# Kernel optimization log

Hardware: AMD Instinct MI355X
Metric: run time of the kernel (lower is better)

## Reference

```python
import jax, jax.numpy as jnp
import numpy as np

IMG = 800.0
STRIDES = (4, 8, 16, 32)
SIZES = (32.0, 64.0, 128.0, 256.0)
RATIOS = (0.5, 1.0, 2.0)
A = 3
PRE_NMS_K = 1000
POST_NMS = 512
NMS_TH = 0.7
POOL = 7
_MEAN = np.array([0.485, 0.456, 0.406], np.float32).reshape(3, 1, 1)
_STD = np.array([0.229, 0.224, 0.225], np.float32).reshape(3, 1, 1)


def _conv(x, w, stride=1):
    # x: [C,H,W], w: [O,I,kh,kw]
    return jax.lax.conv_general_dilated(x[None], w, (stride, stride), 'SAME',
                                        dimension_numbers=('NCHW', 'OIHW', 'NCHW'))[0]


def _make_anchors(fh, fw, stride, size):
    cy = (np.arange(fh, dtype=np.float32) + 0.5) * stride
    cx = (np.arange(fw, dtype=np.float32) + 0.5) * stride
    ws = np.array([size / np.sqrt(r) for r in RATIOS], np.float32)
    hs = np.array([size * np.sqrt(r) for r in RATIOS], np.float32)
    gy, gx = np.meshgrid(cy, cx, indexing='ij')
    x1 = gx[..., None] - ws / 2; y1 = gy[..., None] - hs / 2
    x2 = gx[..., None] + ws / 2; y2 = gy[..., None] + hs / 2
    return jnp.asarray(np.stack([x1, y1, x2, y2], -1).reshape(-1, 4))  # [fh*fw*A,4]


def _decode(anchors, deltas):
    aw = anchors[:, 2] - anchors[:, 0]; ah = anchors[:, 3] - anchors[:, 1]
    acx = anchors[:, 0] + aw * 0.5; acy = anchors[:, 1] + ah * 0.5
    dw = jnp.clip(deltas[:, 2], -4.0, 4.0); dh = jnp.clip(deltas[:, 3], -4.0, 4.0)
    cx = acx + deltas[:, 0] * aw; cy = acy + deltas[:, 1] * ah
    w = aw * jnp.exp(dw); h = ah * jnp.exp(dh)
    boxes = jnp.stack([cx - w * 0.5, cy - h * 0.5, cx + w * 0.5, cy + h * 0.5], -1)
    return jnp.clip(boxes, 0.0, IMG)


def _nms(boxes, scores, iou_th, max_out):
    # Greedy NMS with fixed output size (jit-compatible).
    x1, y1, x2, y2 = boxes[:, 0], boxes[:, 1], boxes[:, 2], boxes[:, 3]
    areas = (x2 - x1) * (y2 - y1)

    def body(i, state):
        s, keep = state
        idx = jnp.argmax(s)
        keep = keep.at[i].set(idx)
        ix1 = jnp.maximum(x1, x1[idx]); iy1 = jnp.maximum(y1, y1[idx])
        ix2 = jnp.minimum(x2, x2[idx]); iy2 = jnp.minimum(y2, y2[idx])
        inter = jnp.maximum(ix2 - ix1, 0.0) * jnp.maximum(iy2 - iy1, 0.0)
        iou = inter / (areas + areas[idx] - inter + 1e-6)
        return jnp.where(iou > iou_th, -jnp.inf, s), keep

    _, keep = jax.lax.fori_loop(0, max_out, body, (scores, jnp.zeros(max_out, jnp.int32)))
    return keep


def _roi_align(feat, rois, scale):
    # feat: [C,H,W]; rois: [N,4] in image coords; bilinear, 1 sample per bin.
    C, H, W = feat.shape
    n = rois.shape[0]
    x1 = rois[:, 0] * scale; y1 = rois[:, 1] * scale
    bw = (rois[:, 2] - rois[:, 0]) * scale / POOL
    bh = (rois[:, 3] - rois[:, 1]) * scale / POOL
    j = jnp.arange(POOL, dtype=feat.dtype) + 0.5
    gx = jnp.broadcast_to((x1[:, None] + j * bw[:, None] - 0.5)[:, None, :], (n, POOL, POOL))
    gy = jnp.broadcast_to((y1[:, None] + j * bh[:, None] - 0.5)[:, :, None], (n, POOL, POOL))
    fx = jnp.clip(jnp.floor(gx), 0.0, W - 1); fy = jnp.clip(jnp.floor(gy), 0.0, H - 1)
    x0 = fx.astype(jnp.int32); y0 = fy.astype(jnp.int32)
    x1i = jnp.minimum(x0 + 1, W - 1); y1i = jnp.minimum(y0 + 1, H - 1)
    wx = jnp.clip(gx - fx, 0.0, 1.0); wy = jnp.clip(gy - fy, 0.0, 1.0)
    v = (feat[:, y0, x0] * (1 - wy) * (1 - wx) + feat[:, y0, x1i] * (1 - wy) * wx
         + feat[:, y1i, x0] * wy * (1 - wx) + feat[:, y1i, x1i] * wy * wx)  # [C,N,P,P]
    return jnp.transpose(v, (1, 0, 2, 3))  # [N,C,P,P]


def _forward(x, stem_w, c2_w, c3_w, c4_w, c5_w, fpn2_w, fpn3_w, fpn4_w, fpn5_w,
             rpn_w, rpn_cls_w, rpn_box_w, fc1_w, fc1_b, fc2_w, fc2_b,
             cls_w, cls_b, breg_w, breg_b):
    x = (x - _MEAN) / _STD  # ImageNet normalize
    h = jax.nn.relu(_conv(x, stem_w, 2))      # [64,400,400]
    c2 = jax.nn.relu(_conv(h, c2_w, 2))       # [256,200,200] stride 4
    c3 = jax.nn.relu(_conv(c2, c3_w, 2))      # stride 8
    c4 = jax.nn.relu(_conv(c3, c4_w, 2))      # stride 16
    c5 = jax.nn.relu(_conv(c4, c5_w, 2))      # stride 32
    feats = [_conv(c2, fpn2_w), _conv(c3, fpn3_w), _conv(c4, fpn4_w), _conv(c5, fpn5_w)]

    boxes_l, scores_l = [], []
    for lvl, f in enumerate(feats):
        t = jax.nn.relu(_conv(f, rpn_w))
        fh, fw = f.shape[1], f.shape[2]
        logits = jnp.transpose(_conv(t, rpn_cls_w), (1, 2, 0)).reshape(-1)  # [fh*fw*A]
        deltas = jnp.transpose(_conv(t, rpn_box_w).reshape(A, 4, fh, fw), (2, 3, 0, 1)).reshape(-1, 4)
        anchors = _make_anchors(fh, fw, STRIDES[lvl], SIZES[lvl])
        dec = _decode(anchors, deltas)
        k = min(PRE_NMS_K, logits.shape[0])
        sc, idx = jax.lax.top_k(logits, k)
        boxes_l.append(dec[idx]); scores_l.append(sc)

    boxes = jnp.concatenate(boxes_l, 0)
    scores = jnp.concatenate(scores_l, 0)
    keep = _nms(boxes, scores, NMS_TH, POST_NMS)
    props = boxes[keep]  # [POST_NMS,4]

    pooled = _roi_align(feats[0], props, 1.0 / STRIDES[0])  # [N,256,7,7]
    v = pooled.reshape(POST_NMS, -1)
    v = jax.nn.relu(v @ fc1_w + fc1_b)
    v = jax.nn.relu(v @ fc2_w + fc2_b)
    return v @ cls_w + cls_b, v @ breg_w + breg_b, props, scores[keep]


def setup_inputs() -> dict:
    key = jax.random.key(0)
    ks = jax.random.split(key, 18)

    def he(k, shape):
        fan_in = int(np.prod(shape[1:])) if len(shape) == 4 else shape[0]
        return jax.random.normal(k, shape, jnp.float32) * float(np.sqrt(2.0 / fan_in))

    inp = {'x': jax.random.uniform(ks[0], (3, 800, 800), jnp.float32)}
    inp['stem_w'] = he(ks[1], (64, 3, 7, 7))
    inp['c2_w'] = he(ks[2], (256, 64, 3, 3))
    for i, name in enumerate(['c3_w', 'c4_w', 'c5_w', 'fpn2_w', 'fpn3_w', 'fpn4_w', 'fpn5_w', 'rpn_w']):
        inp[name] = he(ks[3 + i], (256, 256, 3, 3))
    inp['rpn_cls_w'] = he(ks[11], (3, 256, 1, 1))
    inp['rpn_box_w'] = he(ks[12], (12, 256, 1, 1))
    inp['fc1_w'] = he(ks[13], (12544, 1024)); inp['fc1_b'] = jnp.zeros((1024,), jnp.float32)
    inp['fc2_w'] = he(ks[14], (1024, 1024)); inp['fc2_b'] = jnp.zeros((1024,), jnp.float32)
    inp['cls_w'] = he(ks[15], (1024, 2)); inp['cls_b'] = jnp.zeros((2,), jnp.float32)
    inp['breg_w'] = he(ks[16], (1024, 8)); inp['breg_b'] = jnp.zeros((8,), jnp.float32)
    return inp


def reference(x, stem_w, c2_w, c3_w, c4_w, c5_w, fpn2_w, fpn3_w, fpn4_w, fpn5_w,
              rpn_w, rpn_cls_w, rpn_box_w, fc1_w, fc1_b, fc2_w, fc2_b,
              cls_w, cls_b, breg_w, breg_b):
    return _forward(x, stem_w, c2_w, c3_w, c4_w, c5_w, fpn2_w, fpn3_w, fpn4_w, fpn5_w,
                    rpn_w, rpn_cls_w, rpn_box_w, fc1_w, fc1_b, fc2_w, fc2_b,
                    cls_w, cls_b, breg_w, breg_b)
```

## Files before the change

### kernel.cpp

```cpp
#include <hip/hip_runtime.h>
#include <math.h>


#define DI __device__ __forceinline__

typedef short short8 __attribute__((ext_vector_type(8)));
typedef float float16v __attribute__((ext_vector_type(16)));

DI unsigned fkey(float f) {
  unsigned u = __float_as_uint(f);
  return (u & 0x80000000u) ? ~u : (u | 0x80000000u);
}

DI unsigned short f2bf(float f) {
  unsigned u = __float_as_uint(f);
  unsigned r = (u + 0x7FFFu + ((u >> 16) & 1u)) >> 16;
  return (unsigned short)r;
}

DI void rp256(const float* src, float* dst, int j) {
  int co = j & 15; int r = j >> 4; int kk = r % 9; int r2 = r / 9;
  int ci = r2 & 255; int z = r2 >> 8;
  dst[j] = src[((size_t)(z * 16 + co) * 256 + ci) * 9 + kk];
}
// ... 49 lines not shown
  const int tid = threadIdx.x;
  const int ix0 = x0 * 2 - 2, iy0 = y0 * 2 - 2;
  const float mean[3] = {0.485f, 0.456f, 0.406f};
  const float stdv[3] = {0.229f, 0.224f, 0.225f};
  for (int i = tid; i < 3 * 37 * 37; i += 256) {
    int c = i / 1369, r = i % 1369, yy = r / 37, xx = r % 37;
    int gy = iy0 + yy, gx = ix0 + xx;
    float v = 0.f;
    if ((unsigned)gy < 800u && (unsigned)gx < 800u)
      v = __fdiv_rn(__fsub_rn(x[c * 640000 + gy * 800 + gx], mean[c]), stdv[c]);
    tin[i] = v;
  }
  __syncthreads();
  const int tx = tid & 15, ty = tid >> 4;
  float acc[4] = {0.f, 0.f, 0.f, 0.f};
  const float4* wq = (const float4*)(wpkS + (size_t)blockIdx.z * 588);
  for (int c = 0; c < 3; ++c)
    for (int ky = 0; ky < 7; ++ky)
#pragma unroll
      for (int kx = 0; kx < 7; ++kx) {
        float v = tin[c * 1369 + (ty * 2 + ky) * 37 + (tx * 2 + kx)];
        float4 wv = wq[c * 49 + ky * 7 + kx];
        acc[0] = fmaf(v, wv.x, acc[0]);
        acc[1] = fmaf(v, wv.y, acc[1]);
        acc[2] = fmaf(v, wv.z, acc[2]);
        acc[3] = fmaf(v, wv.w, acc[3]);
      }
  int ox = x0 + tx, oy = y0 + ty;
#pragma unroll
  for (int co = 0; co < 4; ++co)
    out[(size_t)(co0 + co) * 160000 + oy * 400 + ox] = fmaxf(acc[co], 0.f);
}

template <int CHUNK, bool RELU>
DI void conv32_body(const float* __restrict__ in,
                    const float* __restrict__ wpk, float* __restrict__ out,
                    int Cin, int Hin, int Win, int Hout, int Wout, int bx,
                    int by, int bz, float (*tin2)[((CHUNK * 612 + 255) / 256) * 256]) {
  constexpr int TILE = CHUNK * 612;
  constexpr int NS = (TILE + 255) / 256;
  const int tid = threadIdx.x;
  const int tx = tid & 15, ty = tid >> 4;
  const int x0 = bx * 32, y0 = by * 16;
  const int ix0 = x0 - 1, iy0 = y0 - 1;
  const size_t HWin = (size_t)Hin * Win;

  int goff[NS];
#pragma unroll
  for (int j = 0; j < NS; ++j) {
    int e = j * 256 + tid;
    int c = e / 612, r = e % 612;
    int yy = r / 34, xx = r % 34;
    int gy = iy0 + yy, gx = ix0 + xx;
    bool ok = (e < TILE) && ((unsigned)gy < (unsigned)Hin) &&
              ((unsigned)gx < (unsigned)Win);
    goff[j] = ok ? (int)((size_t)c * HWin + (size_t)gy * Win + gx) : -1;
  }

  float acc0[16], acc1[16];
#pragma unroll
  for (int co = 0; co < 16; ++co) { acc0[co] = 0.f; acc1[co] = 0.f; }

  float stg[NS];
#pragma unroll
  for (int j = 0; j < NS; ++j)
    stg[j] = (goff[j] >= 0) ? in[goff[j]] : 0.f;
#pragma unroll
  for (int j = 0; j < NS; ++j) tin2[0][j * 256 + tid] = stg[j];
  __syncthreads();

  int buf = 0;
// ... 39 lines not shown
          acc1[6]  = fmaf(v1, w1.z, acc1[6]);
          acc1[7]  = fmaf(v1, w1.w, acc1[7]);
          acc0[8]  = fmaf(v0, w2.x, acc0[8]);
          acc0[9]  = fmaf(v0, w2.y, acc0[9]);
          acc0[10] = fmaf(v0, w2.z, acc0[10]);
          acc0[11] = fmaf(v0, w2.w, acc0[11]);
          acc1[8]  = fmaf(v1, w2.x, acc1[8]);
          acc1[9]  = fmaf(v1, w2.y, acc1[9]);
          acc1[10] = fmaf(v1, w2.z, acc1[10]);
          acc1[11] = fmaf(v1, w2.w, acc1[11]);
          acc0[12] = fmaf(v0, w3.x, acc0[12]);
          acc0[13] = fmaf(v0, w3.y, acc0[13]);
          acc0[14] = fmaf(v0, w3.z, acc0[14]);
          acc0[15] = fmaf(v0, w3.w, acc0[15]);
          acc1[12] = fmaf(v1, w3.x, acc1[12]);
          acc1[13] = fmaf(v1, w3.y, acc1[13]);
          acc1[14] = fmaf(v1, w3.z, acc1[14]);
          acc1[15] = fmaf(v1, w3.w, acc1[15]);
        }
      }
    }
    if (more) {
#pragma unroll
      for (int j = 0; j < NS; ++j) tin2[buf ^ 1][j * 256 + tid] = stg[j];
    }
    __syncthreads();
    buf ^= 1;
  }

  const int co0 = bz * 16;
  int oy = y0 + ty;
  if (oy < Hout) {
    int ox = x0 + 2 * tx;
    if (ox + 1 < Wout) {
#pragma unroll
      for (int co = 0; co < 16; ++co) {
        float a = acc0[co], b = acc1[co];
        if (RELU) { a = fmaxf(a, 0.f); b = fmaxf(b, 0.f); }
        float2 st; st.x = a; st.y = b;
        *(float2*)&out[(size_t)(co0 + co) * Hout * Wout +
                       (size_t)oy * Wout + ox] = st;
      }
    } else if (ox < Wout) {
#pragma unroll
      for (int co = 0; co < 16; ++co) {
        float a = acc0[co];
        if (RELU) a = fmaxf(a, 0.f);
        out[(size_t)(co0 + co) * Hout * Wout + (size_t)oy * Wout + ox] = a;
      }
    }
  }
}

template <int CHUNK, bool RELU>
__global__ __launch_bounds__(256) void conv32_db(
    const float* __restrict__ in, const float* __restrict__ wpk,
    float* __restrict__ out, int Cin, int Hin, int Win, int Hout, int Wout) {
  constexpr int PADT = ((CHUNK * 612 + 255) / 256) * 256;
  __shared__ __align__(16) float tin2[2][PADT];
  conv32_body<CHUNK, RELU>(in, wpk, out, Cin, Hin, Win, Hout, Wout,
                           blockIdx.x, blockIdx.y, blockIdx.z, tin2);
}

template <int CHUNK>
__global__ __launch_bounds__(256) void conv32_lat(
    const float* __restrict__ inA, const float* __restrict__ wA,
    float* __restrict__ oA, int CinA, int HA, int WA, int gxA, int gyA,
    int nA, const float* __restrict__ inB, const float* __restrict__ wB,
    float* __restrict__ oB, int CinB, int HB, int WB, int gxB, int gyB) {
  constexpr int PADT = ((CHUNK * 612 + 255) / 256) * 256;
  __shared__ __align__(16) float tin2[2][PADT];
  int bid = blockIdx.x;
  if (bid < nA) {
    int bx = bid % gxA; int r = bid / gxA; int by = r % gyA; int bz = r / gyA;
    conv32_body<CHUNK, false>(inA, wA, oA, CinA, HA, WA, HA, WA, bx, by, bz,
                              tin2);
  } else {
    bid -= nA;
    int bx = bid % gxB; int r = bid / gxB; int by = r % gyB; int bz = r / gyB;
    conv32_body<CHUNK, false>(inB, wB, oB, CinB, HB, WB, HB, WB, bx, by, bz,
                              tin2);
  }
}

template <int CHUNK, bool RELU>
DI void conv16s1_body(const float* __restrict__ in,
                      const float* __restrict__ wpk, float* __restrict__ out,
                      int Cin, int Hin, int Win, int Hout, int Wout, int bx,
                      int by, int bz, float* tin) {
  constexpr int P = 24;
  constexpr int TOT = CHUNK * 18 * 18;
  constexpr int NS = (TOT + 255) / 256;
  const int tid = threadIdx.x;
  const int tx = tid & 15, ty = tid >> 4;
  const int x0 = bx * 16, y0 = by * 16;
  const int ix0 = x0 - 1, iy0 = y0 - 1;
  const size_t HWin = (size_t)Hin * Win;

  int goff[NS], loff[NS];
#pragma unroll
  for (int j = 0; j < NS; ++j) {
    int i = tid + j * 256;
    int c = i / 324, r = i % 324;
    int yy = r / 18, xx = r % 18;
    int gy = iy0 + yy, gx = ix0 + xx;
    bool ok = (i < TOT) && ((unsigned)gy < (unsigned)Hin) &&
              ((unsigned)gx < (unsigned)Win);
    goff[j] = ok ? (int)(c * HWin + (size_t)gy * Win + gx) : -1;
    loff[j] = c * 18 * P + yy * P + xx;
  }

  float acc[16];
#pragma unroll
  for (int co = 0; co < 16; ++co) acc[co] = 0.f;

  for (int cb = 0; cb < Cin; cb += CHUNK) {
    const size_t gbase = (size_t)cb * HWin;
#pragma unroll
// ... 13 lines not shown
      for (int ky = 0; ky < 3; ++ky) {
#pragma unroll
        for (int kx = 0; kx < 3; ++kx) {
          const int kk = ky * 3 + kx;
          float v = tin[ci * 18 * P + (ty + ky) * P + tx + kx];
          float4 w0 = wq[kk * 4 + 0];
          float4 w1 = wq[kk * 4 + 1];
          float4 w2 = wq[kk * 4 + 2];
          float4 w3 = wq[kk * 4 + 3];
          acc[0]  = fmaf(v, w0.x, acc[0]);
          acc[1]  = fmaf(v, w0.y, acc[1]);
          acc[2]  = fmaf(v, w0.z, acc[2]);
          acc[3]  = fmaf(v, w0.w, acc[3]);
          acc[4]  = fmaf(v, w1.x, acc[4]);
          acc[5]  = fmaf(v, w1.y, acc[5]);
          acc[6]  = fmaf(v, w1.z, acc[6]);
          acc[7]  = fmaf(v, w1.w, acc[7]);
          acc[8]  = fmaf(v, w2.x, acc[8]);
          acc[9]  = fmaf(v, w2.y, acc[9]);
          acc[10] = fmaf(v, w2.z, acc[10]);
          acc[11] = fmaf(v, w2.w, acc[11]);
          acc[12] = fmaf(v, w3.x, acc[12]);
          acc[13] = fmaf(v, w3.y, acc[13]);
          acc[14] = fmaf(v, w3.z, acc[14]);
          acc[15] = fmaf(v, w3.w, acc[15]);
        }
      }
    }
    __syncthreads();
  }
  const int co0 = bz * 16;
  int oy = y0 + ty, ox = x0 + tx;
  if (oy < Hout && ox < Wout) {
#pragma unroll
    for (int co = 0; co < 16; ++co) {
      float v = acc[co];
      if (RELU) v = fmaxf(v, 0.f);
      out[(size_t)(co0 + co) * Hout * Wout + (size_t)oy * Wout + ox] = v;
    }
  }
}

template <int CHUNK, bool RELU>
__global__ __launch_bounds__(256) void conv16_s1(const float* __restrict__ in,
                                                 const float* __restrict__ wpk,
                                                 float* __restrict__ out,
                                                 int Cin, int Hin, int Win,
                                                 int Hout, int Wout) {
  __shared__ __align__(16) float tin[CHUNK * 18 * 24];
  conv16s1_body<CHUNK, RELU>(in, wpk, out, Cin, Hin, Win, Hout, Wout,
                             blockIdx.x, blockIdx.y, blockIdx.z, tin);
}

template <int CHUNK>
__global__ __launch_bounds__(256) void conv16_lat(
    const float* __restrict__ inA, const float* __restrict__ wA,
    float* __restrict__ oA, int CinA, int HA, int WA, int gxA, int gyA,
    int nA, const float* __restrict__ inB, const float* __restrict__ wB,
    float* __restrict__ oB, int CinB, int HB, int WB, int gxB, int gyB) {
  __shared__ __align__(16) float tin[CHUNK * 18 * 24];
  int bid = blockIdx.x;
  if (bid < nA) {
    int bx = bid % gxA; int r = bid / gxA; int by = r % gyA; int bz = r / gyA;
    conv16s1_body<CHUNK, false>(inA, wA, oA, CinA, HA, WA, HA, WA, bx, by, bz,
                                tin);
  } else {
    bid -= nA;
    int bx = bid % gxB; int r = bid / gxB; int by = r % gyB; int bz = r / gyB;
    conv16s1_body<CHUNK, false>(inB, wB, oB, CinB, HB, WB, HB, WB, bx, by, bz,
                                tin);
  }
}

template <int CHUNK, bool RELU>
__global__ __launch_bounds__(256) void conv16_s2(const float* __restrict__ in,
                                                 const float* __restrict__ wpk,
                                                 float* __restrict__ out,
                                                 int Cin, int Hin, int Win,
                                                 int Hout, int Wout) {
  constexpr int P = 20;
  constexpr int HALF = CHUNK * 33 * P;
  constexpr int TOT = CHUNK * 33 * 33;
  constexpr int NS = (TOT + 255) / 256;
  __shared__ __align__(16) float tin2[2 * HALF];
  const int tid = threadIdx.x;
  const int tx = tid & 15, ty = tid >> 4;
  const int x0 = blockIdx.x * 16, y0 = blockIdx.y * 16;
  const int ix0 = x0 * 2, iy0 = y0 * 2;
  const size_t HWin = (size_t)Hin * Win;

  int goff[NS], loff[NS];
#pragma unroll
  for (int j = 0; j < NS; ++j) {
    int i = tid + j * 256;
    int c = i / 1089, r = i % 1089;
    int yy = r / 33, xx = r % 33;
    int gy = iy0 + yy, gx = ix0 + xx;
    bool ok = (i < TOT) && ((unsigned)gy < (unsigned)Hin) &&
              ((unsigned)gx < (unsigned)Win);
    goff[j] = ok ? (int)(c * HWin + (size_t)gy * Win + gx) : -1;
    loff[j] = c * 33 * P + yy * P + (xx >> 1) + ((xx & 1) ? HALF : 0);
  }

// ... 31 lines not shown
          acc[0]  = fmaf(v, w0.x, acc[0]);
          acc[1]  = fmaf(v, w0.y, acc[1]);
          acc[2]  = fmaf(v, w0.z, acc[2]);
          acc[3]  = fmaf(v, w0.w, acc[3]);
          acc[4]  = fmaf(v, w1.x, acc[4]);
          acc[5]  = fmaf(v, w1.y, acc[5]);
          acc[6]  = fmaf(v, w1.z, acc[6]);
          acc[7]  = fmaf(v, w1.w, acc[7]);
          acc[8]  = fmaf(v, w2.x, acc[8]);
          acc[9]  = fmaf(v, w2.y, acc[9]);
          acc[10] = fmaf(v, w2.z, acc[10]);
          acc[11] = fmaf(v, w2.w, acc[11]);
          acc[12] = fmaf(v, w3.x, acc[12]);
          acc[13] = fmaf(v, w3.y, acc[13]);
          acc[14] = fmaf(v, w3.z, acc[14]);
          acc[15] = fmaf(v, w3.w, acc[15]);
        }
      }
    }
    __syncthreads();
  }
  const int co0 = blockIdx.z * 16;
  int oy = y0 + ty, ox = x0 + tx;
  if (oy < Hout && ox < Wout) {
#pragma unroll
    for (int co = 0; co < 16; ++co) {
      float v = acc[co];
      if (RELU) v = fmaxf(v, 0.f);
      out[(size_t)(co0 + co) * Hout * Wout + (size_t)oy * Wout + ox] = v;
    }
  }
}

__global__ __launch_bounds__(256) void transpose_t(const float* __restrict__ in,
                                                   float* __restrict__ out,
                                                   int npix) {
  __shared__ float tile[32][33];
  const int p0 = blockIdx.x * 32, c0 = blockIdx.y * 32;
  const int tx = threadIdx.x & 31, ty = threadIdx.x >> 5;
  for (int r = ty; r < 32; r += 8) {
    int p = p0 + tx;
    tile[r][tx] = (p < npix) ? in[(size_t)(c0 + r) * npix + p] : 0.f;
  }
  __syncthreads();
  for (int r = ty; r < 32; r += 8) {
    int p = p0 + r;
    if (p < npix) out[(size_t)p * 256 + c0 + tx] = tile[tx][r];
  }
}

__global__ __launch_bounds__(256) void rpn_head_decode(
    const float* __restrict__ tt, const float* __restrict__ wcls,
    const float* __restrict__ wbox, float* __restrict__ boxes,
    float* __restrict__ scores, int fh, int fw, float stride, float ws0,
    float ws1, float ws2, float hs0, float hs1, float hs2) {
  __shared__ __align__(16) float wcs[256][16];
  for (int i = threadIdx.x; i < 256 * 16; i += 256) {
    int c = i & 255, o = i >> 8;
    float v = 0.f;
    if (o < 3) v = wcls[o * 256 + c];
    else if (o < 15) v = wbox[(o - 3) * 256 + c];
    wcs[c][o] = v;
  }
  __syncthreads();
  const int npix = fh * fw;
  int p = blockIdx.x * 256 + threadIdx.x;
  if (p >= npix) return;
  float a[15];
#pragma unroll
  for (int o = 0; o < 15; ++o) a[o] = 0.f;
  const float4* tp = (const float4*)(tt + (size_t)p * 256);
#pragma unroll 4
  for (int c4 = 0; c4 < 64; ++c4) {
    float4 tv = tp[c4];
#pragma unroll
    for (int j = 0; j < 4; ++j) {
      float v = (j == 0) ? tv.x : (j == 1) ? tv.y : (j == 2) ? tv.z : tv.w;
      int c = c4 * 4 + j;
      const float4* wr = (const float4*)&wcs[c][0];
      float4 w0 = wr[0], w1 = wr[1], w2 = wr[2], w3 = wr[3];
      a[0] = fmaf(v, w0.x, a[0]);   a[1] = fmaf(v, w0.y, a[1]);
      a[2] = fmaf(v, w0.z, a[2]);   a[3] = fmaf(v, w0.w, a[3]);
      a[4] = fmaf(v, w1.x, a[4]);   a[5] = fmaf(v, w1.y, a[5]);
      a[6] = fmaf(v, w1.z, a[6]);   a[7] = fmaf(v, w1.w, a[7]);
      a[8] = fmaf(v, w2.x, a[8]);   a[9] = fmaf(v, w2.y, a[9]);
      a[10] = fmaf(v, w2.z, a[10]); a[11] = fmaf(v, w2.w, a[11]);
      a[12] = fmaf(v, w3.x, a[12]); a[13] = fmaf(v, w3.y, a[13]);
      a[14] = fmaf(v, w3.z, a[14]);
    }
  }
  const int i = p / fw, j = p % fw;
  const float acy0 = __fmul_rn((float)i + 0.5f, stride);
  const float acx0 = __fmul_rn((float)j + 0.5f, stride);
  const float WS[3] = {ws0, ws1, ws2}, HS[3] = {hs0, hs1, hs2};
#pragma unroll
  for (int an = 0; an < 3; ++an) {
    float hw = __fmul_rn(WS[an], 0.5f), hh = __fmul_rn(HS[an], 0.5f);
    float x1a = __fsub_rn(acx0, hw), x2a = __fadd_rn(acx0, hw);
    float y1a = __fsub_rn(acy0, hh), y2a = __fadd_rn(acy0, hh);
    float aw = __fsub_rn(x2a, x1a), ah = __fsub_rn(y2a, y1a);
    float acx = __fadd_rn(x1a, __fmul_rn(aw, 0.5f));
    float acy = __fadd_rn(y1a, __fmul_rn(ah, 0.5f));
    float dx = a[3 + an * 4 + 0], dy = a[3 + an * 4 + 1];
    float dw = fminf(fmaxf(a[3 + an * 4 + 2], -4.f), 4.f);
    float dh = fminf(fmaxf(a[3 + an * 4 + 3], -4.f), 4.f);
    float cx = __fadd_rn(acx, __fmul_rn(dx, aw));
    float cy = __fadd_rn(acy, __fmul_rn(dy, ah));
    float w_ = __fmul_rn(aw, expf(dw));
    float h_ = __fmul_rn(ah, expf(dh));
    int idx = p * 3 + an;
    boxes[idx * 4 + 0] =
        fminf(fmaxf(__fsub_rn(cx, __fmul_rn(w_, 0.5f)), 0.f), 800.f);
    boxes[idx * 4 + 1] =
        fminf(fmaxf(__fsub_rn(cy, __fmul_rn(h_, 0.5f)), 0.f), 800.f);
    boxes[idx * 4 + 2] =
        fminf(fmaxf(__fadd_rn(cx, __fmul_rn(w_, 0.5f)), 0.f), 800.f);
    boxes[idx * 4 + 3] =
        fminf(fmaxf(__fadd_rn(cy, __fmul_rn(h_, 0.5f)), 0.f), 800.f);
    scores[idx] = a[an];
  }
}

__global__ void hist_hi_kernel(const float* __restrict__ s, int n,
                               int* __restrict__ hist) {
  int i = blockIdx.x * blockDim.x + threadIdx.x;
  if (i < n) atomicAdd(&hist[fkey(s[i]) >> 16], 1);
}

__global__ void hist_lo_kernel(const float* __restrict__ s, int n,
                               const int* __restrict__ sel,
                               int* __restrict__ hist) {
  unsigned b = (unsigned)sel[0];
  int i = blockIdx.x * blockDim.x + threadIdx.x;
  if (i < n) {
    unsigned key = fkey(s[i]);
    if ((key >> 16) == b) atomicAdd(&hist[key & 0xffffu], 1);
  }
}

__global__ __launch_bounds__(256) void scan_hi_kernel(
    const int* __restrict__ hist, int k, int* __restrict__ sel) {
  __shared__ int csum[256];
  int t = threadIdx.x;
  int s = 0;
  for (int i = 0; i < 256; ++i) s += hist[t * 256 + i];
  csum[t] = s;
  __syncthreads();
  if (t == 0) {
    int cum = 0;
    for (int c = 255; c >= 0; --c) {
      if (cum + csum[c] >= k) {
        int cc = cum;
        for (int b = c * 256 + 255;; --b) {
          int h = hist[b];
          if (cc + h >= k) {
            sel[0] = b; sel[1] = k - cc; sel[2] = cc;
            return;
          }
          cc += h;
        }
      }
      cum += csum[c];
    }
    sel[0] = 0; sel[1] = k - cum; sel[2] = cum;
  }
}

__global__ __launch_bounds__(256) void scan_lo_kernel(
    const int* __restrict__ hist, int* __restrict__ sel) {
  __shared__ int csum[256];
  int t = threadIdx.x;
  int s = 0;
  for (int i = 0; i < 256; ++i) s += hist[t * 256 + i];
  csum[t] = s;
  __syncthreads();
  if (t == 0) {
    int r = sel[1], b = sel[0], cc_hi = sel[2];
    int cum = 0;
    for (int c = 255; c >= 0; --c) {
      if (cum + csum[c] >= r) {
        int cc = cum;
        for (int l = c * 256 + 255;; --l) {
          int h = hist[l];
          if (cc + h >= r) {
            sel[3] = (int)(((unsigned)b << 16) | (unsigned)l);
            sel[4] = cc_hi + cc;
            sel[5] = r - cc;
            sel[6] = 0;
            sel[7] = 0;
            return;
          }
          cc += h;
        }
      }
      cum += csum[c];
    }
    sel[3] = (int)((unsigned)b << 16);
    sel[4] = cc_hi; sel[5] = r; sel[6] = 0; sel[7] = 0;
  }
}

__global__ void compact_kernel(const float* __restrict__ s,
                               const float* __restrict__ boxes, int n,
                               int* __restrict__ sel, float* __restrict__ out_s,
                               float* __restrict__ out_b, int obase) {
  int i = blockIdx.x * blockDim.x + threadIdx.x;
  if (i >= n) return;
  unsigned key = fkey(s[i]);
  unsigned kth = (unsigned)sel[3];
  int pos = -1;
  if (key > kth) {
    pos = atomicAdd(&sel[6], 1);
  } else if (key == kth) {
    int e = atomicAdd(&sel[7], 1);
    if (e < sel[5]) pos = sel[4] + e;
  }
  if (pos >= 0) {
    int o = obase + pos;
    out_s[o] = s[i];
    out_b[o * 4 + 0] = boxes[i * 4 + 0];
    out_b[o * 4 + 1] = boxes[i * 4 + 1];
    out_b[o * 4 + 2] = boxes[i * 4 + 2];
    out_b[o * 4 + 3] = boxes[i * 4 + 3];
  }
}

#define NMS_N 4000
#define NMS_W 63

__global__ __launch_bounds__(256) void rank_kernel(const float* __restrict__ s,
                                                   int* __restrict__ order) {
  __shared__ float ls[NMS_N];
  for (int i = threadIdx.x; i < NMS_N; i += 256) ls[i] = s[i];
  __syncthreads();
  int i = blockIdx.x * 256 + threadIdx.x;
  if (i >= NMS_N) return;
  float si = ls[i];
  int cnt = 0;
  for (int j = 0; j < NMS_N; ++j) {
    float sj = ls[j];
    cnt += (sj > si) || (sj == si && j < i);
  }
  order[cnt] = i;
}

__global__ __launch_bounds__(256) void supp_kernel(
    const float* __restrict__ boxes, unsigned long long* __restrict__ supp) {
  __shared__ float sx1[NMS_W * 64], sy1[NMS_W * 64];
  __shared__ float sx2[NMS_W * 64], sy2[NMS_W * 64];
  for (int i = threadIdx.x; i < NMS_W * 64; i += 256) {
    float x1 = 0.f, y1 = 0.f, x2 = 0.f, y2 = 0.f;
    if (i < NMS_N) {
      x1 = boxes[i * 4 + 0]; y1 = boxes[i * 4 + 1];
      x2 = boxes[i * 4 + 2]; y2 = boxes[i * 4 + 3];
    }
    sx1[i] = x1; sy1[i] = y1; sx2[i] = x2; sy2[i] = y2;
// ... 201 lines not shown
  const float* w_c3   = (const float*)d_in[3];
  const float* w_c4   = (const float*)d_in[4];
  const float* w_c5   = (const float*)d_in[5];
  const float* w_f2   = (const float*)d_in[6];
  const float* w_f3   = (const float*)d_in[7];
  const float* w_f4   = (const float*)d_in[8];
  const float* w_f5   = (const float*)d_in[9];
  const float* w_rpn  = (const float*)d_in[10];
  const float* w_cls  = (const float*)d_in[11];
  const float* w_box  = (const float*)d_in[12];
  const float* w_fc1  = (const float*)d_in[13];
  const float* b_fc1  = (const float*)d_in[14];
  const float* w_fc2  = (const float*)d_in[15];
  const float* b_fc2  = (const float*)d_in[16];
  const float* w_clsh = (const float*)d_in[17];
  const float* b_clsh = (const float*)d_in[18];
  const float* w_breg = (const float*)d_in[19];
  const float* b_breg = (const float*)d_in[20];
  float* dout = (float*)d_out;

  float* ws = (float*)d_ws;
  float* stem = ws;
  float* c2   = stem + 10240000;
  float* c3   = c2 + 10240000;
  float* c4   = c3 + 2560000;
  float* c5   = c4 + 640000;
  float* f2   = c5 + 160000;
  float* f3   = f2 + 10240000;
  float* f4   = f3 + 2560000;
  float* f5   = f4 + 640000;
  float* boxes_all  = f5 + 160000;
  float* scores_all = boxes_all + 16000;
  float* props      = scores_all + 4000;
  int*   hist = (int*)(props + 2048);
  int*   sel  = hist + 65536;
  float* wpkA = (float*)(sel + 16);
  float* wpkB = wpkA + 589824;
  float* wpkC = wpkB + 589824;
  float* wpkD = wpkC + 589824;
  float* wpkE = wpkD + 147456;
  float* wpkF = wpkE + 589824;
  float* wpkG = wpkF + 589824;
  float* wpkH = wpkG + 589824;
  float* wpkI = wpkH + 589824;
  float* wpkS = wpkI + 589824;
  float* t      = c2;
  float* tt     = stem;
  float* dec    = c3;
  float* slvl   = c4;
  int*   order  = (int*)c3;
  unsigned long long* supp =
      (unsigned long long*)(c3 + 8192);
  float* pooled = stem;
  float* fc1o   = stem + 6422528;
  float* fc2o   = fc1o + 524288;
  float* fcp    = fc2o + 524288;
  unsigned short* Abf1 = (unsigned short*)c2;
  unsigned short* Bt1  = (unsigned short*)(c2 + 3211264);
  unsigned short* Abf2 = (unsigned short*)c3;
  unsigned short* Bt2  = (unsigned short*)(c3 + 262144);

  repack_all<<<19045, 256, 0, stream>>>(
      w_f2, w_f3, w_rpn, w_c2, w_c3, w_c4, w_c5, w_f4, w_f5, w_stem,
      wpkA, wpkB, wpkC, wpkD, wpkE, wpkF, wpkG, wpkH, wpkI, wpkS);

  stem_conv<<<dim3(25, 25, 16), 256, 0, stream>>>(x, wpkS, stem);
  conv16_s2<4, true><<<dim3(13, 13, 16), 256, 0, stream>>>(
      stem, wpkD, c2, 64, 400, 400, 200, 200);
  conv16_s2<4, true><<<dim3(7, 7, 16), 256, 0, stream>>>(
      c2, wpkE, c3, 256, 200, 200, 100, 100);
  conv16_s2<4, true><<<dim3(4, 4, 16), 256, 0, stream>>>(
      c3, wpkF, c4, 256, 100, 100, 50, 50);
  conv16_s2<4, true><<<dim3(2, 2, 16), 256, 0, stream>>>(
      c4, wpkG, c5, 256, 50, 50, 25, 25);
  conv32_lat<4><<<1904, 256, 0, stream>>>(
      c2, wpkA, f2, 256, 200, 200, 7, 13, 1456,
      c3, wpkB, f3, 256, 100, 100, 4, 7);
  conv16_lat<8><<<320, 256, 0, stream>>>(
      c4, wpkH, f4, 256, 50, 50, 4, 4, 256,
      c5, wpkI, f5, 256, 25, 25, 2, 2);

  const float* feats[4] = {f2, f3, f4, f5};
  const int dims[4] = {200, 100, 50, 25};
  const float strds[4] = {4.f, 8.f, 16.f, 32.f};
  const double szs[4] = {32.0, 64.0, 128.0, 256.0};
  for (int lvl = 0; lvl < 4; ++lvl) {
    const int d = dims[lvl];
    const int npix = d * d;
    const int N = npix * 3;
    if (lvl == 0)
      conv32_db<4, true><<<dim3(7, 13, 16), 256, 0, stream>>>(
          feats[lvl], wpkC, t, 256, d, d, d, d);
    else if (lvl == 1)
      conv32_db<4, true><<<dim3(4, 7, 16), 256, 0, stream>>>(
          feats[lvl], wpkC, t, 256, d, d, d, d);
    else if (lvl == 2)
      conv16_s1<8, true><<<dim3(4, 4, 16), 256, 0, stream>>>(
          feats[lvl], wpkC, t, 256, d, d, d, d);
    else
      conv16_s1<8, true><<<dim3(2, 2, 16), 256, 0, stream>>>(
          feats[lvl], wpkC, t, 256, d, d, d, d);
    transpose_t<<<dim3((npix + 31) / 32, 8), 256, 0, stream>>>(t, tt, npix);
    double sz = szs[lvl];
    float ws0 = (float)(sz / sqrt(0.5)), ws1 = (float)sz,
          ws2 = (float)(sz / sqrt(2.0));
    float hs0 = (float)(sz * sqrt(0.5)), hs1 = (float)sz,
          hs2 = (float)(sz * sqrt(2.0));
    rpn_head_decode<<<(npix + 255) / 256, 256, 0, stream>>>(
        tt, w_cls, w_box, dec, slvl, d, d, strds[lvl], ws0, ws1, ws2, hs0, hs1,
        hs2);
    hipMemsetAsync(hist, 0, 65536 * sizeof(int), stream);
    hist_hi_kernel<<<(N + 255) / 256, 256, 0, stream>>>(slvl, N, hist);
    scan_hi_kernel<<<1, 256, 0, stream>>>(hist, 1000, sel);
    hipMemsetAsync(hist, 0, 65536 * sizeof(int), stream);
    hist_lo_kernel<<<(N + 255) / 256, 256, 0, stream>>>(slvl, N, sel, hist);
    scan_lo_kernel<<<1, 256, 0, stream>>>(hist, sel);
    compact_kernel<<<(N + 255) / 256, 256, 0, stream>>>(
        slvl, dec, N, sel, scores_all, boxes_all, lvl * 1000);
  }

  rank_kernel<<<16, 256, 0, stream>>>(scores_all, order);
  supp_kernel<<<250, 256, 0, stream>>>(boxes_all, supp);
  nms_scan<<<1, 64, 0, stream>>>(supp, order, boxes_all, scores_all, props,
                                 dout + 5120, dout + 7168);

  roi_align_kernel<<<512, 256, 0, stream>>>(f2, props, pooled);
  cast_a<<<(6422528 + 255) / 256, 256, 0, stream>>>(pooled, Abf1, 6422528);
  cast_bt<<<dim3(32, 392), 256, 0, stream>>>(w_fc1, Bt1, 12544, 1024);
  fc_mfma<<<dim3(16, 4, 4), 256, 0, stream>>>(Abf1, Bt1, fcp, 512, 1024, 12544,
                                              3136);
  fc_combine<<<2048, 256, 0, stream>>>(fcp, b_fc1, fc1o, 524288, 1024, 4);
  cast_a<<<(524288 + 255) / 256, 256, 0, stream>>>(fc1o, Abf2, 524288);
  cast_bt<<<dim3(32, 32), 256, 0, stream>>>(w_fc2, Bt2, 1024, 1024);
  fc_mfma<<<dim3(16, 4, 4), 256, 0, stream>>>(Abf2, Bt2, fcp, 512, 1024, 1024,
                                              256);
  fc_combine<<<2048, 256, 0, stream>>>(fcp, b_fc2, fc2o, 524288, 1024, 4);
  heads_kernel<<<512, 64, 0, stream>>>(fc2o, w_clsh, b_clsh, w_breg, b_breg,
                                       dout);
}
```

Measured before the change: 4.935 ms.

## Batch RPN levels into single launches with channel-last conv output and fused histogram

Runs the shared RPN 3x3 conv for all four FPN levels as two batched launches that write pixel-major (channel-last) output directly, which removes the separate transpose kernels. The decode for all levels becomes one kernel that also builds the high-half score histogram with atomics. The histogram scans, low-half histogram and compaction each run once over all levels instead of once per level. This cuts roughly thirty small serial launches and memsets down to a handful. The cost is strided 16-float scattered stores in the conv epilogue and more buffer aliasing of scratch regions, which could break correctness.

Measured after the change: 4.406 ms. 1.12x faster.

```diff
diff --git a/kernel.cpp b/kernel.cpp
--- a/kernel.cpp
+++ b/kernel.cpp
@@ -105,11 +105,12 @@
     out[(size_t)(co0 + co) * 160000 + oy * 400 + ox] = fmaxf(acc[co], 0.f);
 }
 
-template <int CHUNK, bool RELU>
+template <int CHUNK, bool RELU, bool TT>
 DI void conv32_body(const float* __restrict__ in,
                     const float* __restrict__ wpk, float* __restrict__ out,
                     int Cin, int Hin, int Win, int Hout, int Wout, int bx,
-                    int by, int bz, float (*tin2)[((CHUNK * 612 + 255) / 256) * 256]) {
+                    int by, int bz,
+                    float (*tin2)[((CHUNK * 612 + 255) / 256) * 256]) {
   constexpr int TILE = CHUNK * 612;
   constexpr int NS = (TILE + 255) / 256;
   const int tid = threadIdx.x;
@@ -215,37 +216,48 @@
   int oy = y0 + ty;
   if (oy < Hout) {
     int ox = x0 + 2 * tx;
-    if (ox + 1 < Wout) {
-#pragma unroll
-      for (int co = 0; co < 16; ++co) {
-        float a = acc0[co], b = acc1[co];
-        if (RELU) { a = fmaxf(a, 0.f); b = fmaxf(b, 0.f); }
-        float2 st; st.x = a; st.y = b;
-        *(float2*)&out[(size_t)(co0 + co) * Hout * Wout +
-                       (size_t)oy * Wout + ox] = st;
-      }
-    } else if (ox < Wout) {
-#pragma unroll
-      for (int co = 0; co < 16; ++co) {
-        float a = acc0[co];
-        if (RELU) a = fmaxf(a, 0.f);
-        out[(size_t)(co0 + co) * Hout * Wout + (size_t)oy * Wout + ox] = a;
-      }
-    }
-  }
-}
-
-template <int CHUNK, bool RELU>
-__global__ __launch_bounds__(256) void conv32_db(
-    const float* __restrict__ in, const float* __restrict__ wpk,
-    float* __restrict__ out, int Cin, int Hin, int Win, int Hout, int Wout) {
-  constexpr int PADT = ((CHUNK * 612 + 255) / 256) * 256;
-  __shared__ __align__(16) float tin2[2][PADT];
-  conv32_body<CHUNK, RELU>(in, wpk, out, Cin, Hin, Win, Hout, Wout,
-                           blockIdx.x, blockIdx.y, blockIdx.z, tin2);
-}
-
-template <int CHUNK>
+    if (TT) {
+      if (ox < Wout) {
+        float* o = out + (size_t)(oy * Wout + ox) * 256 + co0;
+#pragma unroll
+        for (int co = 0; co < 16; ++co) {
+          float a = acc0[co];
+          if (RELU) a = fmaxf(a, 0.f);
+          o[co] = a;
+        }
+      }
+      if (ox + 1 < Wout) {
+        float* o = out + (size_t)(oy * Wout + ox + 1) * 256 + co0;
+#pragma unroll
+        for (int co = 0; co < 16; ++co) {
+          float a = acc1[co];
+          if (RELU) a = fmaxf(a, 0.f);
+          o[co] = a;
+        }
+      }
+    } else {
+      if (ox + 1 < Wout) {
+#pragma unroll
+        for (int co = 0; co < 16; ++co) {
+          float a = acc0[co], b = acc1[co];
+          if (RELU) { a = fmaxf(a, 0.f); b = fmaxf(b, 0.f); }
+          float2 st; st.x = a; st.y = b;
+          *(float2*)&out[(size_t)(co0 + co) * Hout * Wout +
+                         (size_t)oy * Wout + ox] = st;
+        }
+      } else if (ox < Wout) {
+#pragma unroll
+        for (int co = 0; co < 16; ++co) {
+          float a = acc0[co];
+          if (RELU) a = fmaxf(a, 0.f);
+          out[(size_t)(co0 + co) * Hout * Wout + (size_t)oy * Wout + ox] = a;
+        }
+      }
+    }
+  }
+}
+
+template <int CHUNK, bool RELU, bool TT>
 __global__ __launch_bounds__(256) void conv32_lat(
     const float* __restrict__ inA, const float* __restrict__ wA,
     float* __restrict__ oA, int CinA, int HA, int WA, int gxA, int gyA,
@@ -256,17 +268,17 @@
   int bid = blockIdx.x;
   if (bid < nA) {
     int bx = bid % gxA; int r = bid / gxA; int by = r % gyA; int bz = r / gyA;
-    conv32_body<CHUNK, false>(inA, wA, oA, CinA, HA, WA, HA, WA, bx, by, bz,
-                              tin2);
+    conv32_body<CHUNK, RELU, TT>(inA, wA, oA, CinA, HA, WA, HA, WA, bx, by,
+                                 bz, tin2);
   } else {
     bid -= nA;
     int bx = bid % gxB; int r = bid / gxB; int by = r % gyB; int bz = r / gyB;
-    conv32_body<CHUNK, false>(inB, wB, oB, CinB, HB, WB, HB, WB, bx, by, bz,
-                              tin2);
-  }
-}
-
-template <int CHUNK, bool RELU>
+    conv32_body<CHUNK, RELU, TT>(inB, wB, oB, CinB, HB, WB, HB, WB, bx, by,
+                                 bz, tin2);
+  }
+}
+
+template <int CHUNK, bool RELU, bool TT>
 DI void conv16s1_body(const float* __restrict__ in,
                       const float* __restrict__ wpk, float* __restrict__ out,
                       int Cin, int Hin, int Win, int Hout, int Wout, int bx,
@@ -346,27 +358,26 @@
   const int co0 = bz * 16;
   int oy = y0 + ty, ox = x0 + tx;
   if (oy < Hout && ox < Wout) {
-#pragma unroll
-    for (int co = 0; co < 16; ++co) {
-      float v = acc[co];
-      if (RELU) v = fmaxf(v, 0.f);
-      out[(size_t)(co0 + co) * Hout * Wout + (size_t)oy * Wout + ox] = v;
-    }
-  }
-}
-
-template <int CHUNK, bool RELU>
-__global__ __launch_bounds__(256) void conv16_s1(const float* __restrict__ in,
-                                                 const float* __restrict__ wpk,
-                                                 float* __restrict__ out,
-                                                 int Cin, int Hin, int Win,
-                                                 int Hout, int Wout) {
-  __shared__ __align__(16) float tin[CHUNK * 18 * 24];
-  conv16s1_body<CHUNK, RELU>(in, wpk, out, Cin, Hin, Win, Hout, Wout,
-                             blockIdx.x, blockIdx.y, blockIdx.z, tin);
-}
-
-template <int CHUNK>
+    if (TT) {
+      float* o = out + (size_t)(oy * Wout + ox) * 256 + co0;
+#pragma unroll
+      for (int co = 0; co < 16; ++co) {
+        float v = acc[co];
+        if (RELU) v = fmaxf(v, 0.f);
+        o[co] = v;
+      }
+    } else {
+#pragma unroll
+      for (int co = 0; co < 16; ++co) {
+        float v = acc[co];
+        if (RELU) v = fmaxf(v, 0.f);
+        out[(size_t)(co0 + co) * Hout * Wout + (size_t)oy * Wout + ox] = v;
+      }
+    }
+  }
+}
+
+template <int CHUNK, bool RELU, bool TT>
 __global__ __launch_bounds__(256) void conv16_lat(
     const float* __restrict__ inA, const float* __restrict__ wA,
     float* __restrict__ oA, int CinA, int HA, int WA, int gxA, int gyA,
@@ -376,13 +387,13 @@
   int bid = blockIdx.x;
   if (bid < nA) {
     int bx = bid % gxA; int r = bid / gxA; int by = r % gyA; int bz = r / gyA;
-    conv16s1_body<CHUNK, false>(inA, wA, oA, CinA, HA, WA, HA, WA, bx, by, bz,
-                                tin);
+    conv16s1_body<CHUNK, RELU, TT>(inA, wA, oA, CinA, HA, WA, HA, WA, bx, by,
+                                   bz, tin);
   } else {
     bid -= nA;
     int bx = bid % gxB; int r = bid / gxB; int by = r % gyB; int bz = r / gyB;
-    conv16s1_body<CHUNK, false>(inB, wB, oB, CinB, HB, WB, HB, WB, bx, by, bz,
-                                tin);
+    conv16s1_body<CHUNK, RELU, TT>(inB, wB, oB, CinB, HB, WB, HB, WB, bx, by,
+                                   bz, tin);
   }
 }
 
@@ -480,28 +491,12 @@
   }
 }
 
-__global__ __launch_bounds__(256) void transpose_t(const float* __restrict__ in,
-                                                   float* __restrict__ out,
-                                                   int npix) {
-  __shared__ float tile[32][33];
-  const int p0 = blockIdx.x * 32, c0 = blockIdx.y * 32;
-  const int tx = threadIdx.x & 31, ty = threadIdx.x >> 5;
-  for (int r = ty; r < 32; r += 8) {
-    int p = p0 + tx;
-    tile[r][tx] = (p < npix) ? in[(size_t)(c0 + r) * npix + p] : 0.f;
-  }
-  __syncthreads();
-  for (int r = ty; r < 32; r += 8) {
-    int p = p0 + r;
-    if (p < npix) out[(size_t)p * 256 + c0 + tx] = tile[tx][r];
-  }
-}
-
-__global__ __launch_bounds__(256) void rpn_head_decode(
-    const float* __restrict__ tt, const float* __restrict__ wcls,
-    const float* __restrict__ wbox, float* __restrict__ boxes,
-    float* __restrict__ scores, int fh, int fw, float stride, float ws0,
-    float ws1, float ws2, float hs0, float hs1, float hs2) {
+__global__ __launch_bounds__(256) void rpn_decode_all(
+    const float* __restrict__ tt0, const float* __restrict__ tt1,
+    const float* __restrict__ tt2, const float* __restrict__ tt3,
+    const float* __restrict__ wcls, const float* __restrict__ wbox,
+    float* __restrict__ boxes4, float* __restrict__ scores4,
+    int* __restrict__ hist4) {
   __shared__ __align__(16) float wcs[256][16];
   for (int i = threadIdx.x; i < 256 * 16; i += 256) {
     int c = i & 255, o = i >> 8;
@@ -511,9 +506,28 @@
     wcs[c][o] = v;
   }
   __syncthreads();
-  const int npix = fh * fw;
-  int p = blockIdx.x * 256 + threadIdx.x;
+  int b = blockIdx.x;
+  int lvl; int base, npix, fw, boff, soff; float stride; const float* tt;
+  if (b < 157) {
+    lvl = 0; base = 0; npix = 40000; fw = 200; boff = 0; soff = 0;
+    stride = 4.f; tt = tt0;
+  } else if (b < 197) {
+    lvl = 1; base = 157; npix = 10000; fw = 100; boff = 480000;
+    soff = 120000; stride = 8.f; tt = tt1;
+  } else if (b < 207) {
+    lvl = 2; base = 197; npix = 2500; fw = 50; boff = 600000;
+    soff = 150000; stride = 16.f; tt = tt2;
+  } else {
+    lvl = 3; base = 207; npix = 625; fw = 25; boff = 630000;
+    soff = 157500; stride = 32.f; tt = tt3;
+  }
+  int p = (b - base) * 256 + threadIdx.x;
   if (p >= npix) return;
+  double sz = (double)(32 << lvl);
+  float ws0 = (float)(sz / sqrt(0.5)), ws1 = (float)sz,
+        ws2 = (float)(sz / sqrt(2.0));
+  float hs0 = (float)(sz * sqrt(0.5)), hs1 = (float)sz,
+        hs2 = (float)(sz * sqrt(2.0));
   float a[15];
 #pragma unroll
   for (int o = 0; o < 15; ++o) a[o] = 0.f;
@@ -557,38 +571,26 @@
     float w_ = __fmul_rn(aw, expf(dw));
     float h_ = __fmul_rn(ah, expf(dh));
     int idx = p * 3 + an;
-    boxes[idx * 4 + 0] =
+    float* bo = boxes4 + boff;
+    bo[idx * 4 + 0] =
         fminf(fmaxf(__fsub_rn(cx, __fmul_rn(w_, 0.5f)), 0.f), 800.f);
-    boxes[idx * 4 + 1] =
+    bo[idx * 4 + 1] =
         fminf(fmaxf(__fsub_rn(cy, __fmul_rn(h_, 0.5f)), 0.f), 800.f);
-    boxes[idx * 4 + 2] =
+    bo[idx * 4 + 2] =
         fminf(fmaxf(__fadd_rn(cx, __fmul_rn(w_, 0.5f)), 0.f), 800.f);
-    boxes[idx * 4 + 3] =
+    bo[idx * 4 + 3] =
         fminf(fmaxf(__fadd_rn(cy, __fmul_rn(h_, 0.5f)), 0.f), 800.f);
-    scores[idx] = a[an];
-  }
-}
-
-__global__ void hist_hi_kernel(const float* __restrict__ s, int n,
-                               int* __restrict__ hist) {
-  int i = blockIdx.x * blockDim.x + threadIdx.x;
-  if (i < n) atomicAdd(&hist[fkey(s[i]) >> 16], 1);
-}
-
-__global__ void hist_lo_kernel(const float* __restrict__ s, int n,
-                               const int* __restrict__ sel,
-                               int* __restrict__ hist) {
-  unsigned b = (unsigned)sel[0];
-  int i = blockIdx.x * blockDim.x + threadIdx.x;
-  if (i < n) {
-    unsigned key = fkey(s[i]);
-    if ((key >> 16) == b) atomicAdd(&hist[key & 0xffffu], 1);
-  }
-}
-
-__global__ __launch_bounds__(256) void scan_hi_kernel(
-    const int* __restrict__ hist, int k, int* __restrict__ sel) {
+    scores4[soff + idx] = a[an];
+    atomicAdd(&hist4[lvl * 65536 + (fkey(a[an]) >> 16)], 1);
+  }
+}
+
+__global__ __launch_bounds__(256) void scan_hi_all(int* __restrict__ hist4,
+                                                   int* __restrict__ sel4) {
   __shared__ int csum[256];
+  int* hist = hist4 + blockIdx.x * 65536;
+  int* sel = sel4 + blockIdx.x * 8;
+  const int k = 1000;
   int t = threadIdx.x;
   int s = 0;
   for (int i = 0; i < 256; ++i) s += hist[t * 256 + i];
@@ -596,6 +598,7 @@
   __syncthreads();
   if (t == 0) {
     int cum = 0;
+    bool done = false;
     for (int c = 255; c >= 0; --c) {
       if (cum + csum[c] >= k) {
         int cc = cum;
@@ -603,20 +606,49 @@
           int h = hist[b];
           if (cc + h >= k) {
             sel[0] = b; sel[1] = k - cc; sel[2] = cc;
-            return;
+            done = true;
+            break;
           }
           cc += h;
         }
+        break;
       }
       cum += csum[c];
     }
-    sel[0] = 0; sel[1] = k - cum; sel[2] = cum;
-  }
-}
-
-__global__ __launch_bounds__(256) void scan_lo_kernel(
-    const int* __restrict__ hist, int* __restrict__ sel) {
+    if (!done) { sel[0] = 0; sel[1] = k - cum; sel[2] = cum; }
+  }
+  __syncthreads();
+  int4 z4; z4.x = 0; z4.y = 0; z4.z = 0; z4.w = 0;
+  for (int i = t; i < 16384; i += 256) ((int4*)hist)[i] = z4;
+}
+
+DI void lvl_seg(int b, int& lvl, int& base, int& N, int& soff, int& boff) {
+  if (b < 469) { lvl = 0; base = 0; N = 120000; soff = 0; boff = 0; }
+  else if (b < 587) { lvl = 1; base = 469; N = 30000; soff = 120000;
+                      boff = 480000; }
+  else if (b < 617) { lvl = 2; base = 587; N = 7500; soff = 150000;
+                      boff = 600000; }
+  else { lvl = 3; base = 617; N = 1875; soff = 157500; boff = 630000; }
+}
+
+__global__ void hist_lo_all(const float* __restrict__ scores4,
+                            const int* __restrict__ sel4,
+                            int* __restrict__ hist4) {
+  int lvl, base, N, soff, boff;
+  lvl_seg(blockIdx.x, lvl, base, N, soff, boff);
+  int i = (blockIdx.x - base) * 256 + threadIdx.x;
+  if (i >= N) return;
+  unsigned bsel = (unsigned)sel4[lvl * 8 + 0];
+  unsigned key = fkey(scores4[soff + i]);
+  if ((key >> 16) == bsel)
+    atomicAdd(&hist4[lvl * 65536 + (key & 0xffffu)], 1);
+}
+
+__global__ __launch_bounds__(256) void scan_lo_all(
+    const int* __restrict__ hist4, int* __restrict__ sel4) {
   __shared__ int csum[256];
+  const int* hist = hist4 + blockIdx.x * 65536;
+  int* sel = sel4 + blockIdx.x * 8;
   int t = threadIdx.x;
   int s = 0;
   for (int i = 0; i < 256; ++i) s += hist[t * 256 + i];
@@ -625,6 +657,7 @@
   if (t == 0) {
     int r = sel[1], b = sel[0], cc_hi = sel[2];
     int cum = 0;
+    bool done = false;
     for (int c = 255; c >= 0; --c) {
       if (cum + csum[c] >= r) {
         int cc = cum;
@@ -636,25 +669,33 @@
             sel[5] = r - cc;
             sel[6] = 0;
             sel[7] = 0;
-            return;
+            done = true;
+            break;
           }
           cc += h;
         }
+        break;
       }
       cum += csum[c];
     }
-    sel[3] = (int)((unsigned)b << 16);
-    sel[4] = cc_hi; sel[5] = r; sel[6] = 0; sel[7] = 0;
-  }
-}
-
-__global__ void compact_kernel(const float* __restrict__ s,
-                               const float* __restrict__ boxes, int n,
-                               int* __restrict__ sel, float* __restrict__ out_s,
-                               float* __restrict__ out_b, int obase) {
-  int i = blockIdx.x * blockDim.x + threadIdx.x;
-  if (i >= n) return;
-  unsigned key = fkey(s[i]);
+    if (!done) {
+      sel[3] = (int)((unsigned)b << 16);
+      sel[4] = cc_hi; sel[5] = r; sel[6] = 0; sel[7] = 0;
+    }
+  }
+}
+
+__global__ void compact_all(const float* __restrict__ scores4,
+                            const float* __restrict__ boxes4,
+                            int* __restrict__ sel4,
+                            float* __restrict__ out_s,
+                            float* __restrict__ out_b) {
+  int lvl, base, N, soff, boff;
+  lvl_seg(blockIdx.x, lvl, base, N, soff, boff);
+  int i = (blockIdx.x - base) * 256 + threadIdx.x;
+  if (i >= N) return;
+  int* sel = sel4 + lvl * 8;
+  unsigned key = fkey(scores4[soff + i]);
   unsigned kth = (unsigned)sel[3];
   int pos = -1;
   if (key > kth) {
@@ -664,12 +705,13 @@
     if (e < sel[5]) pos = sel[4] + e;
   }
   if (pos >= 0) {
-    int o = obase + pos;
-    out_s[o] = s[i];
-    out_b[o * 4 + 0] = boxes[i * 4 + 0];
-    out_b[o * 4 + 1] = boxes[i * 4 + 1];
-    out_b[o * 4 + 2] = boxes[i * 4 + 2];
-    out_b[o * 4 + 3] = boxes[i * 4 + 3];
+    int o = lvl * 1000 + pos;
+    out_s[o] = scores4[soff + i];
+    const float* bo = boxes4 + boff;
+    out_b[o * 4 + 0] = bo[i * 4 + 0];
+    out_b[o * 4 + 1] = bo[i * 4 + 1];
+    out_b[o * 4 + 2] = bo[i * 4 + 2];
+    out_b[o * 4 + 3] = bo[i * 4 + 3];
   }
 }
 
@@ -937,8 +979,8 @@
   float* boxes_all  = f5 + 160000;
   float* scores_all = boxes_all + 16000;
   float* props      = scores_all + 4000;
-  int*   hist = (int*)(props + 2048);
-  int*   sel  = hist + 65536;
+  int*   histOld = (int*)(props + 2048);
+  int*   sel  = histOld + 65536;
   float* wpkA = (float*)(sel + 16);
   float* wpkB = wpkA + 589824;
   float* wpkC = wpkB + 589824;
@@ -949,10 +991,14 @@
   float* wpkH = wpkG + 589824;
   float* wpkI = wpkH + 589824;
   float* wpkS = wpkI + 589824;
-  float* t      = c2;
-  float* tt     = stem;
-  float* dec    = c3;
-  float* slvl   = c4;
+  float* tt0 = stem;
+  float* tt1 = c3;
+  float* tt2 = wpkF;
+  float* tt3 = wpkH;
+  int*   hist4 = (int*)wpkE;
+  int*   sel4  = histOld;
+  float* boxes4  = c4;
+  float* scores4 = c5;
   int*   order  = (int*)c3;
   unsigned long long* supp =
       (unsigned long long*)(c3 + 8192);
@@ -978,51 +1024,28 @@
       c3, wpkF, c4, 256, 100, 100, 50, 50);
   conv16_s2<4, true><<<dim3(2, 2, 16), 256, 0, stream>>>(
       c4, wpkG, c5, 256, 50, 50, 25, 25);
-  conv32_lat<4><<<1904, 256, 0, stream>>>(
+  conv32_lat<4, false, false><<<1904, 256, 0, stream>>>(
       c2, wpkA, f2, 256, 200, 200, 7, 13, 1456,
       c3, wpkB, f3, 256, 100, 100, 4, 7);
-  conv16_lat<8><<<320, 256, 0, stream>>>(
+  conv16_lat<8, false, false><<<320, 256, 0, stream>>>(
       c4, wpkH, f4, 256, 50, 50, 4, 4, 256,
       c5, wpkI, f5, 256, 25, 25, 2, 2);
 
-  const float* feats[4] = {f2, f3, f4, f5};
-  const int dims[4] = {200, 100, 50, 25};
-  const float strds[4] = {4.f, 8.f, 16.f, 32.f};
-  const double szs[4] = {32.0, 64.0, 128.0, 256.0};
-  for (int lvl = 0; lvl < 4; ++lvl) {
-    const int d = dims[lvl];
-    const int npix = d * d;
-    const int N = npix * 3;
-    if (lvl == 0)
-      conv32_db<4, true><<<dim3(7, 13, 16), 256, 0, stream>>>(
-          feats[lvl], wpkC, t, 256, d, d, d, d);
-    else if (lvl == 1)
-      conv32_db<4, true><<<dim3(4, 7, 16), 256, 0, stream>>>(
-          feats[lvl], wpkC, t, 256, d, d, d, d);
-    else if (lvl == 2)
-      conv16_s1<8, true><<<dim3(4, 4, 16), 256, 0, stream>>>(
-          feats[lvl], wpkC, t, 256, d, d, d, d);
-    else
-      conv16_s1<8, true><<<dim3(2, 2, 16), 256, 0, stream>>>(
-          feats[lvl], wpkC, t, 256, d, d, d, d);
-    transpose_t<<<dim3((npix + 31) / 32, 8), 256, 0, stream>>>(t, tt, npix);
-    double sz = szs[lvl];
-    float ws0 = (float)(sz / sqrt(0.5)), ws1 = (float)sz,
-          ws2 = (float)(sz / sqrt(2.0));
-    float hs0 = (float)(sz * sqrt(0.5)), hs1 = (float)sz,
-          hs2 = (float)(sz * sqrt(2.0));
-    rpn_head_decode<<<(npix + 255) / 256, 256, 0, stream>>>(
-        tt, w_cls, w_box, dec, slvl, d, d, strds[lvl], ws0, ws1, ws2, hs0, hs1,
-        hs2);
-    hipMemsetAsync(hist, 0, 65536 * sizeof(int), stream);
-    hist_hi_kernel<<<(N + 255) / 256, 256, 0, stream>>>(slvl, N, hist);
-    scan_hi_kernel<<<1, 256, 0, stream>>>(hist, 1000, sel);
-    hipMemsetAsync(hist, 0, 65536 * sizeof(int), stream);
-    hist_lo_kernel<<<(N + 255) / 256, 256, 0, stream>>>(slvl, N, sel, hist);
-    scan_lo_kernel<<<1, 256, 0, stream>>>(hist, sel);
-    compact_kernel<<<(N + 255) / 256, 256, 0, stream>>>(
-        slvl, dec, N, sel, scores_all, boxes_all, lvl * 1000);
-  }
+  conv32_lat<4, true, true><<<1904, 256, 0, stream>>>(
+      f2, wpkC, tt0, 256, 200, 200, 7, 13, 1456,
+      f3, wpkC, tt1, 256, 100, 100, 4, 7);
+  conv16_lat<8, true, true><<<320, 256, 0, stream>>>(
+      f4, wpkC, tt2, 256, 50, 50, 4, 4, 256,
+      f5, wpkC, tt3, 256, 25, 25, 2, 2);
+
+  hipMemsetAsync(hist4, 0, 4 * 65536 * sizeof(int), stream);
+  rpn_decode_all<<<210, 256, 0, stream>>>(tt0, tt1, tt2, tt3, w_cls, w_box,
+                                          boxes4, scores4, hist4);
+  scan_hi_all<<<4, 256, 0, stream>>>(hist4, sel4);
+  hist_lo_all<<<625, 256, 0, stream>>>(scores4, sel4, hist4);
+  scan_lo_all<<<4, 256, 0, stream>>>(hist4, sel4);
+  compact_all<<<625, 256, 0, stream>>>(scores4, boxes4, sel4, scores_all,
+                                       boxes_all);
 
   rank_kernel<<<16, 256, 0, stream>>>(scores_all, order);
   supp_kernel<<<250, 256, 0, stream>>>(boxes_all, supp);
```
